# Kernel tuning notes

Hardware: AMD Instinct MI355X
Metric: run time of the kernel (lower is better)

Reference implementation:

```python
import jax, jax.numpy as jnp
import numpy as np

HEADS = 4
HEAD_DIM = 32
NUM_GRAPHS = 512


def _transformer_conv(x, Wq, bq, Wk, bk, Wv, bv, Ws, bs, src, dst):
    # PyG TransformerConv, concat=False, root_weight=True, beta=False, eval mode (no dropout).
    N = x.shape[0]
    q = (x @ Wq + bq).reshape(N, HEADS, HEAD_DIM)
    k = (x @ Wk + bk).reshape(N, HEADS, HEAD_DIM)
    v = (x @ Wv + bv).reshape(N, HEADS, HEAD_DIM)
    scale = 1.0 / np.sqrt(HEAD_DIM).astype(np.float32)
    # per-edge attention logits: query at target (dst), key at source (src)
    logits = jnp.einsum('ehd,ehd->eh', q[dst], k[src]) * scale  # [E, H]
    # segment softmax over incoming edges of each target node
    m = jax.ops.segment_max(logits, dst, num_segments=N)        # [N, H]
    p = jnp.exp(logits - m[dst])                                # [E, H]
    denom = jax.ops.segment_sum(p, dst, num_segments=N)         # [N, H]
    a = p / jnp.maximum(denom[dst], 1e-16)                      # [E, H]
    msg = a[:, :, None] * v[src]                                # [E, H, D]
    out = jax.ops.segment_sum(msg, dst, num_segments=N)         # [N, H, D]
    out = out.mean(axis=1)                                      # concat=False -> head mean
    return out + (x @ Ws + bs)                                  # root/skip connection


def _global_mean_pool(x, batch, num_graphs):
    s = jax.ops.segment_sum(x, batch, num_segments=num_graphs)
    cnt = jax.ops.segment_sum(jnp.ones((x.shape[0],), x.dtype), batch, num_segments=num_graphs)
    return s / jnp.maximum(cnt, 1.0)[:, None]


def setup_inputs() -> dict:
    key = jax.random.key(0)
    ks = jax.random.split(key, 20)
    N, E, C, H = 100000, 1600000, 128, 32
    d = {
        'x': jax.random.normal(ks[0], (N, C), jnp.float32),
        'edge_index': jax.random.randint(ks[1], (2, E), 0, N, jnp.int64),
        'batch': jnp.sort(jax.random.randint(ks[2], (N,), 0, NUM_GRAPHS, jnp.int64)),
    }
    def lin(k, fan_in, fan_out):
        lim = 1.0 / np.sqrt(fan_in)
        k1, k2 = jax.random.split(k)
        return (jax.random.uniform(k1, (fan_in, fan_out), jnp.float32, -lim, lim),
                jax.random.uniform(k2, (fan_out,), jnp.float32, -lim, lim))
    d['Wq1'], d['bq1'] = lin(ks[3], C, HEADS * HEAD_DIM)
    d['Wk1'], d['bk1'] = lin(ks[4], C, HEADS * HEAD_DIM)
    d['Wv1'], d['bv1'] = lin(ks[5], C, HEADS * HEAD_DIM)
    d['Ws1'], d['bs1'] = lin(ks[6], C, H)
    d['Wq2'], d['bq2'] = lin(ks[7], H, HEADS * HEAD_DIM)
    d['Wk2'], d['bk2'] = lin(ks[8], H, HEADS * HEAD_DIM)
    d['Wv2'], d['bv2'] = lin(ks[9], H, HEADS * HEAD_DIM)
    d['Ws2'], d['bs2'] = lin(ks[10], H, H)
    return d


def reference(x, edge_index, batch, Wq1, bq1, Wk1, bk1, Wv1, bv1, Ws1, bs1,
              Wq2, bq2, Wk2, bk2, Wv2, bv2, Ws2, bs2):
    src, dst = edge_index[0], edge_index[1]
    h = _transformer_conv(x, Wq1, bq1, Wk1, bk1, Wv1, bv1, Ws1, bs1, src, dst)
    h = jax.nn.relu(h)
    h = _transformer_conv(h, Wq2, bq2, Wk2, bk2, Wv2, bv2, Ws2, bs2, src, dst)
    h = jax.nn.relu(h)
    return _global_mean_pool(h, batch, NUM_GRAPHS)
```

## Files before the change

### kernel.cpp

```cpp
#include <hip/hip_runtime.h>
#include <math.h>

typedef __attribute__((ext_vector_type(8))) short bf16x8;
typedef __attribute__((ext_vector_type(4))) float f32x4;

__device__ __forceinline__ float b2f(unsigned short u) {
    union { unsigned u32; float f; } x; x.u32 = (unsigned)u << 16; return x.f;
}
__device__ __forceinline__ unsigned short f2b(float f) {
    union { float f; unsigned u32; } x; x.f = f;
    unsigned u = x.u32;
    unsigned r = (u + 0x7fffu + ((u >> 16) & 1u)) >> 16;
    return (unsigned short)r;
}

__device__ __forceinline__ unsigned char f2e4m3(float f) {
    union { float f; unsigned u; } x; x.f = f;
    unsigned s = (x.u >> 24) & 0x80;
    x.u &= 0x7fffffff;
    if (!(x.f == x.f)) return (unsigned char)(s | 0x7e);
    if (x.f >= 448.f) return (unsigned char)(s | 0x7e);
    if (x.f < 0.015625f) {
        int m = (int)rintf(x.f * 512.f);
        if (m >= 8) return (unsigned char)(s | 0x08);
        return (unsigned char)(s | (unsigned)m);
    }
    unsigned exp = x.u >> 23;
    unsigned mant = x.u & 0x7fffff;
    unsigned m3 = mant >> 20;
    unsigned rb = (mant >> 19) & 1u;
    unsigned sticky = (mant & 0x7ffffu) ? 1u : 0u;
    m3 += rb & (sticky | (m3 & 1u));
    if (m3 == 8) { m3 = 0; exp++; }
    unsigned e4 = exp - 120;
    if (e4 >= 15 && m3 > 6) { e4 = 15; m3 = 6; }
    return (unsigned char)(s | (e4 << 3) | m3);
}

__device__ __forceinline__ void acc4_fp8(float exs, unsigned vw, float4& acc) {
    union { unsigned u; float f; } t;
    t.u = ((vw & 0x80u) << 24) | ((vw & 0x7fu) << 20);        acc.x += exs * t.f;
    t.u = ((vw & 0x8000u) << 16) | ((vw & 0x7f00u) << 12);    acc.y += exs * t.f;
    t.u = ((vw & 0x800000u) << 8) | ((vw & 0x7f0000u) << 4);  acc.z += exs * t.f;
    t.u = (vw & 0x80000000u) | ((vw & 0x7f000000u) >> 4);     acc.w += exs * t.f;
}

__device__ __forceinline__ f32x4 mfma16(bf16x8 a, bf16x8 b, f32x4 c) {
    return __builtin_amdgcn_mfma_f32_16x16x32_bf16(a, b, c, 0, 0, 0);
}

__device__ __forceinline__ void async_copy16(const unsigned* g, void* l) {
    __builtin_amdgcn_global_load_lds(
        (const __attribute__((address_space(1))) unsigned*)g,
        (__attribute__((address_space(3))) unsigned*)l, 16, 0, 0);
}


__global__ __launch_bounds__(256) void hist_k(const int* __restrict__ dst, int* __restrict__ deg, int E) {
    int e = blockIdx.x * 256 + threadIdx.x;
    if (e < E) atomicAdd(&deg[dst[e]], 1);
}

__global__ __launch_bounds__(256) void scanA_k(const int* __restrict__ deg, int* __restrict__ rowptr,
                                               int* __restrict__ partials, int N) {
    __shared__ int sh[256];
    int t = threadIdx.x;
    int base = blockIdx.x * 1024 + t * 4;
    int v0 = 0, v1 = 0, v2 = 0, v3 = 0;
    if (base + 0 < N) v0 = deg[base + 0];
    if (base + 1 < N) v1 = deg[base + 1];
    if (base + 2 < N) v2 = deg[base + 2];
    if (base + 3 < N) v3 = deg[base + 3];
    sh[t] = v0 + v1 + v2 + v3;
    __syncthreads();
    for (int off = 1; off < 256; off <<= 1) {
        int add = (t >= off) ? sh[t - off] : 0;
        __syncthreads();
        sh[t] += add;
        __syncthreads();
    }
    int run = (t > 0) ? sh[t - 1] : 0;
    if (base + 0 < N) rowptr[base + 0] = run; run += v0;
    if (base + 1 < N) rowptr[base + 1] = run; run += v1;
    if (base + 2 < N) rowptr[base + 2] = run; run += v2;
    if (base + 3 < N) rowptr[base + 3] = run;
    if (t == 255) partials[blockIdx.x] = sh[255];
}

__global__ void scanB_k(int* partials, int nch) {
    if (threadIdx.x == 0 && blockIdx.x == 0) {
        int run = 0;
        for (int i = 0; i < nch; ++i) { int x = partials[i]; partials[i] = run; run += x; }
        partials[nch] = run;
    }
}

__global__ __launch_bounds__(256) void addoff_k(int* __restrict__ rowptr, const int* __restrict__ partials,
                                                int N, int nch) {
    int t = threadIdx.x;
    int off = partials[blockIdx.x];
    int base = blockIdx.x * 1024;
    for (int i = 0; i < 4; ++i) {
        int idx = base + t + i * 256;
        if (idx < N) rowptr[idx] += off;
    }
    if (blockIdx.x == 0 && t == 0) rowptr[N] = partials[nch];
}

__global__ __launch_bounds__(256) void scatter_k(const int* __restrict__ src, const int* __restrict__ dst,
                                                 const int* __restrict__ rowptr, int* __restrict__ cnt,
                                                 int* __restrict__ srcid, int E) {
    int e = blockIdx.x * 256 + threadIdx.x;
    if (e < E) {
        int d = dst[e];
        int pos = rowptr[d] + atomicAdd(&cnt[d], 1);
        srcid[pos] = src[e];
    }
}


__global__ __launch_bounds__(256) void cvt_k(const float* __restrict__ x,
                                             unsigned short* __restrict__ hi,
                                             unsigned short* __restrict__ lo, long n4) {
    long stride = (long)gridDim.x * 256;
    for (long i = (long)blockIdx.x * 256 + threadIdx.x; i < n4; i += stride) {
        float4 v = ((const float4*)x)[i];
        ushort4 h, L;
        h.x = f2b(v.x); L.x = f2b(v.x - b2f(h.x));
        h.y = f2b(v.y); L.y = f2b(v.y - b2f(h.y));
        h.z = f2b(v.z); L.z = f2b(v.z - b2f(h.z));
        h.w = f2b(v.w); L.w = f2b(v.w - b2f(h.w));
        ((ushort4*)hi)[i] = h;
        ((ushort4*)lo)[i] = L;
    }
}


__global__ __launch_bounds__(256) void wprep_k(
    const float* __restrict__ Wq, const float* __restrict__ Wk,
    const float* __restrict__ Wv, const float* __restrict__ Ws,
    int ksteps, unsigned* __restrict__ fhi, unsigned* __restrict__ flo)
{
    int idx = blockIdx.x * 256 + threadIdx.x;
    int total = 26 * ksteps * 64 * 4;
    if (idx >= total) return;
    int w = idx & 3;
    int lane = (idx >> 2) & 63;
    int tmp = idx >> 8;
    int kk = tmp % ksteps;
    int t = tmp / ksteps;
    int col = t * 16 + (lane & 15);
    int k0 = kk * 32 + ((lane >> 4) << 3) + (w << 1);
    const float* W; int ow, c;
    if (col < 128)      { W = Wq; ow = 128; c = col; }
    else if (col < 256) { W = Wk; ow = 128; c = col - 128; }
    else if (col < 384) { W = Wv; ow = 128; c = col - 256; }
    else                { W = Ws; ow = 32;  c = col - 384; }
    float v0 = W[(size_t)k0 * ow + c];
    float v1 = W[(size_t)(k0 + 1) * ow + c];
    unsigned short h0 = f2b(v0), h1 = f2b(v1);
    unsigned short l0 = f2b(v0 - b2f(h0)), l1 = f2b(v1 - b2f(h1));
    fhi[idx] = (unsigned)h0 | ((unsigned)h1 << 16);
    flo[idx] = (unsigned)l0 | ((unsigned)l1 << 16);
}


template<int KSTEPS>
__global__ __launch_bounds__(1024) void qkvs_mfma(const unsigned short* __restrict__ Xhi,
    const unsigned short* __restrict__ Xlo, int Cin, int N,
    const unsigned* __restrict__ fhi, const unsigned* __restrict__ flo,
    const float* __restrict__ bq, const float* __restrict__ bk,
    const float* __restrict__ bv, const float* __restrict__ bs,
    unsigned short* __restrict__ q, unsigned char* __restrict__ kvb,
    float* __restrict__ sk, int rtPer)
{
    constexpr int NT = 7;
    constexpr int NIDX = KSTEPS * NT * 2 * 64;
    __shared__ float4 ldsB[NIDX];

    int tid = threadIdx.x;
    int lane = tid & 63, wid = tid >> 6;
    int tbase = blockIdx.y * NT;

    for (int u = tid; u < NIDX; u += 1024) {
        int l = u & 63;
        int rest = u >> 6;
        int plane = rest & 1;
        int tt = (rest >> 1) % NT;
        int kk = (rest >> 1) / NT;
        if (tbase + tt < 26) {
            const unsigned* srcp = plane ? flo : fhi;
            size_t so = (((size_t)(tbase + tt) * KSTEPS + kk) * 64 + l) * 4;
            async_copy16(srcp + so, &ldsB[u - l]);
        }
    }
    __syncthreads();

    const int asub = (lane >> 4) << 3;
    int rtTotal = (N + 15) >> 4;
    int rtStart = blockIdx.x * rtPer;
    int rtEnd = rtStart + rtPer; if (rtEnd > rtTotal) rtEnd = rtTotal;

    for (int rt = rtStart + wid; rt < rtEnd; rt += 16) {
        int row = rt * 16 + (lane & 15);
        int rowc = row < N ? row : N - 1;
        const unsigned short* xh = Xhi + (size_t)rowc * Cin + asub;
        const unsigned short* xl = Xlo + (size_t)rowc * Cin + asub;

        f32x4 acc[NT];
#pragma unroll
        for (int t = 0; t < NT; ++t) acc[t] = (f32x4){0.f, 0.f, 0.f, 0.f};

        bf16x8 ah = *(const bf16x8*)xh;
        bf16x8 al = *(const bf16x8*)xl;
#pragma unroll
        for (int kk = 0; kk < KSTEPS; ++kk) {
            bf16x8 ahn, aln;
            if (kk + 1 < KSTEPS) {
                ahn = *(const bf16x8*)(xh + (kk + 1) * 32);
                aln = *(const bf16x8*)(xl + (kk + 1) * 32);
            }
            const float4* base = &ldsB[kk * NT * 2 * 64];
#pragma unroll
            for (int t = 0; t < NT; ++t) {
                bf16x8 bh = *(const bf16x8*)&base[(t * 2 + 0) * 64 + lane];
                bf16x8 bl = *(const bf16x8*)&base[(t * 2 + 1) * 64 + lane];
                acc[t] = mfma16(ah, bh, acc[t]);
                acc[t] = mfma16(al, bh, acc[t]);
                acc[t] = mfma16(ah, bl, acc[t]);
            }
            if (kk + 1 < KSTEPS) { ah = ahn; al = aln; }
        }

#pragma unroll
        for (int t = 0; t < NT; ++t) {
            int col = (tbase + t) * 16 + (lane & 15);
            if (col >= 416) continue;
            int sel; const float* bp; int c;
            if (col < 128)      { sel = 0; bp = bq; c = col; }
            else if (col < 256) { sel = 1; bp = bk; c = col - 128; }
            else if (col < 384) { sel = 2; bp = bv; c = col - 256; }
            else                { sel = 3; bp = bs; c = col - 384; }
            float bias = bp[c];
#pragma unroll
            for (int r = 0; r < 4; ++r) {
                int orow = rt * 16 + ((lane >> 4) << 2) + r;
                if (orow >= N) continue;
                float val = acc[t][r] + bias;
                if (sel == 0)      q[(size_t)orow * 128 + c] = f2b(val);
                else if (sel == 1) *(unsigned short*)(kvb + (size_t)orow * 384 + c * 2) = f2b(val);
                else if (sel == 2) kvb[(size_t)orow * 384 + 256 + c] = f2e4m3(val);
                else               sk[(size_t)orow * 32 + c] = val;
            }
        }
    }
}


__global__ __launch_bounds__(256) void attn_k(const unsigned short* __restrict__ q,
    const unsigned char* __restrict__ kv,
    const float* __restrict__ sk,
    const int* __restrict__ rowptr, const int* __restrict__ srcid,
    float* __restrict__ outF, unsigned short* __restrict__ outHi,
    unsigned short* __restrict__ outLo, int mode, int N)
{
    int grp = threadIdx.x >> 5;
    int n = blockIdx.x * 8 + grp;
    if (n >= N) return;
    int l = threadIdx.x & 31;
    int s = l & 7;
    const float c2 = 0.25504233001306574f;

    ushort4 qr = *(const ushort4*)(q + (size_t)n * 128 + l * 4);
    float4 qv = make_float4(b2f(qr.x), b2f(qr.y), b2f(qr.z), b2f(qr.w));
    float4 acc = make_float4(0.f, 0.f, 0.f, 0.f);
    float lsum = 0.f;

    int e0 = rowptr[n], e1 = rowptr[n + 1];
    int e = e0;
    for (; e + 4 <= e1; e += 4) {
        int s0 = srcid[e], s1 = srcid[e + 1], s2 = srcid[e + 2], s3 = srcid[e + 3];
        const unsigned char* b0 = kv + (size_t)s0 * 384;
        const unsigned char* b1 = kv + (size_t)s1 * 384;
        const unsigned char* b2 = kv + (size_t)s2 * 384;
        const unsigned char* b3 = kv + (size_t)s3 * 384;
        ushort4 k0 = *(const ushort4*)(b0 + (l << 3));
        ushort4 k1 = *(const ushort4*)(b1 + (l << 3));
        ushort4 k2 = *(const ushort4*)(b2 + (l << 3));
        ushort4 k3 = *(const ushort4*)(b3 + (l << 3));
        unsigned vw0 = *(const unsigned*)(b0 + 256 + (l << 2));
        unsigned vw1 = *(const unsigned*)(b1 + 256 + (l << 2));
        unsigned vw2 = *(const unsigned*)(b2 + 256 + (l << 2));
        unsigned vw3 = *(const unsigned*)(b3 + 256 + (l << 2));

        float p0 = qv.x * b2f(k0.x) + qv.y * b2f(k0.y) + qv.z * b2f(k0.z) + qv.w * b2f(k0.w);
        float p1 = qv.x * b2f(k1.x) + qv.y * b2f(k1.y) + qv.z * b2f(k1.z) + qv.w * b2f(k1.w);
        float p2 = qv.x * b2f(k2.x) + qv.y * b2f(k2.y) + qv.z * b2f(k2.z) + qv.w * b2f(k2.w);
        float p3 = qv.x * b2f(k3.x) + qv.y * b2f(k3.y) + qv.z * b2f(k3.z) + qv.w * b2f(k3.w);
        p0 += __shfl_xor(p0, 1, 8); p0 += __shfl_xor(p0, 2, 8); p0 += __shfl_xor(p0, 4, 8);
        p1 += __shfl_xor(p1, 1, 8); p1 += __shfl_xor(p1, 2, 8); p1 += __shfl_xor(p1, 4, 8);
        p2 += __shfl_xor(p2, 1, 8); p2 += __shfl_xor(p2, 2, 8); p2 += __shfl_xor(p2, 4, 8);
        p3 += __shfl_xor(p3, 1, 8); p3 += __shfl_xor(p3, 2, 8); p3 += __shfl_xor(p3, 4, 8);
        float ex0 = exp2f(fminf(p0 * c2, 86.f));
        float ex1 = exp2f(fminf(p1 * c2, 86.f));
        float ex2 = exp2f(fminf(p2 * c2, 86.f));
        float ex3 = exp2f(fminf(p3 * c2, 86.f));
        lsum += (ex0 + ex1) + (ex2 + ex3);
        acc4_fp8(ex0 * 0x1p120f, vw0, acc);
        acc4_fp8(ex1 * 0x1p120f, vw1, acc);
        acc4_fp8(ex2 * 0x1p120f, vw2, acc);
        acc4_fp8(ex3 * 0x1p120f, vw3, acc);
    }
    for (; e < e1; ++e) {
        const unsigned char* b0 = kv + (size_t)srcid[e] * 384;
        ushort4 k0 = *(const ushort4*)(b0 + (l << 3));
        unsigned vw0 = *(const unsigned*)(b0 + 256 + (l << 2));
        float p0 = qv.x * b2f(k0.x) + qv.y * b2f(k0.y) + qv.z * b2f(k0.z) + qv.w * b2f(k0.w);
        p0 += __shfl_xor(p0, 1, 8); p0 += __shfl_xor(p0, 2, 8); p0 += __shfl_xor(p0, 4, 8);
        float ex0 = exp2f(fminf(p0 * c2, 86.f));
        lsum += ex0;
        acc4_fp8(ex0 * 0x1p120f, vw0, acc);
    }

    float inv = 0.25f / fmaxf(lsum, 1e-16f);
    float rx = acc.x * inv, ry = acc.y * inv, rz = acc.z * inv, rw = acc.w * inv;
    rx += __shfl_xor(rx, 8, 32);  rx += __shfl_xor(rx, 16, 32);
    ry += __shfl_xor(ry, 8, 32);  ry += __shfl_xor(ry, 16, 32);
    rz += __shfl_xor(rz, 8, 32);  rz += __shfl_xor(rz, 16, 32);
    rw += __shfl_xor(rw, 8, 32);  rw += __shfl_xor(rw, 16, 32);

    if (l < 8) {
        const float* skp = sk + (size_t)n * 32 + s * 4;
        float o0 = fmaxf(rx + skp[0], 0.f), o1 = fmaxf(ry + skp[1], 0.f);
        float o2 = fmaxf(rz + skp[2], 0.f), o3 = fmaxf(rw + skp[3], 0.f);
        if (mode == 0) {
            *(float4*)(outF + (size_t)n * 32 + s * 4) = make_float4(o0, o1, o2, o3);
        } else {
            ushort4 h, L;
            h.x = f2b(o0); L.x = f2b(o0 - b2f(h.x));
            h.y = f2b(o1); L.y = f2b(o1 - b2f(h.y));
            h.z = f2b(o2); L.z = f2b(o2 - b2f(h.z));
            h.w = f2b(o3); L.w = f2b(o3 - b2f(h.w));
            *(ushort4*)(outHi + (size_t)n * 32 + s * 4) = h;
            *(ushort4*)(outLo + (size_t)n * 32 + s * 4) = L;
        }
    }
}


__global__ __launch_bounds__(256) void pool_k(const float* __restrict__ h, const int* __restrict__ batch,
                                              float* __restrict__ out, int N)
{
    int g = blockIdx.x;
    int t = threadIdx.x;
    int lo = 0, hi = N;
    while (lo < hi) { int mid = (lo + hi) >> 1; if (batch[mid] < g) lo = mid + 1; else hi = mid; }
    int start = lo;
    lo = 0; hi = N;
    while (lo < hi) { int mid = (lo + hi) >> 1; if (batch[mid] < g + 1) lo = mid + 1; else hi = mid; }
    int end = lo;
    int c = t & 31, r0 = t >> 5;
    float s = 0.f;
    for (int r = start + r0; r < end; r += 8) s += h[(size_t)r * 32 + c];
    __shared__ float sh[256];
    sh[t] = s;
    __syncthreads();
    if (t < 32) {
        float tot = sh[t] + sh[t + 32] + sh[t + 64] + sh[t + 96]
                  + sh[t + 128] + sh[t + 160] + sh[t + 192] + sh[t + 224];
        float cnt = (float)(end - start);
        out[(size_t)g * 32 + t] = tot / fmaxf(cnt, 1.f);
    }
}


extern "C" void kernel_launch(void* const* d_in, const int* in_sizes, int n_in,
                              void* d_out, int out_size, void* d_ws, size_t ws_size,
                              hipStream_t stream) {
    const float* x   = (const float*)d_in[0];
    const int* ei    = (const int*)d_in[1];
    const int* batch = (const int*)d_in[2];
    const float *Wq1 = (const float*)d_in[3],  *bq1 = (const float*)d_in[4];
    const float *Wk1 = (const float*)d_in[5],  *bk1 = (const float*)d_in[6];
    const float *Wv1 = (const float*)d_in[7],  *bv1 = (const float*)d_in[8];
    const float *Ws1 = (const float*)d_in[9],  *bs1 = (const float*)d_in[10];
    const float *Wq2 = (const float*)d_in[11], *bq2 = (const float*)d_in[12];
    const float *Wk2 = (const float*)d_in[13], *bk2 = (const float*)d_in[14];
    const float *Wv2 = (const float*)d_in[15], *bv2 = (const float*)d_in[16];
    const float *Ws2 = (const float*)d_in[17], *bs2 = (const float*)d_in[18];
    float* out = (float*)d_out;

    int N = in_sizes[0] / 128;
    int E = in_sizes[1] / 2;
    const int* src = ei;
    const int* dst = ei + E;

    char* ws = (char*)d_ws;
    size_t off = 0;
    auto alloc = [&](size_t bytes) -> void* {
        void* p = ws + off;
        off += (bytes + 255) & ~(size_t)255;
        return p;
    };
    int* deg      = (int*)alloc((size_t)N * 4);
    int* cnt      = (int*)alloc((size_t)N * 4);
    int* rowptr   = (int*)alloc(((size_t)N + 1) * 4);
    int* partials = (int*)alloc(4096);
    int* srcid    = (int*)alloc((size_t)E * 4);
    unsigned* fhi1 = (unsigned*)alloc(26 * 4 * 64 * 4 * 4);
    unsigned* flo1 = (unsigned*)alloc(26 * 4 * 64 * 4 * 4);
    unsigned* fhi2 = (unsigned*)alloc(26 * 1 * 64 * 4 * 4);
    unsigned* flo2 = (unsigned*)alloc(26 * 1 * 64 * 4 * 4);
    unsigned short* Xhi = (unsigned short*)alloc((size_t)N * 128 * 2);
    unsigned short* Xlo = (unsigned short*)alloc((size_t)N * 128 * 2);
    unsigned short* q   = (unsigned short*)alloc((size_t)N * 128 * 2);
    unsigned char* kvb  = (unsigned char*)alloc((size_t)N * 384);
    float* sk     = (float*)alloc((size_t)N * 32 * 4);
    unsigned short* h1hi = (unsigned short*)alloc((size_t)N * 32 * 2);
    unsigned short* h1lo = (unsigned short*)alloc((size_t)N * 32 * 2);
    float* h2     = (float*)alloc((size_t)N * 32 * 4);

    hipMemsetAsync(deg, 0, (size_t)N * 4, stream);
    hipMemsetAsync(cnt, 0, (size_t)N * 4, stream);

    int nch = (N + 1023) / 1024;
    hist_k<<<(E + 255) / 256, 256, 0, stream>>>(dst, deg, E);
    scanA_k<<<nch, 256, 0, stream>>>(deg, rowptr, partials, N);
    scanB_k<<<1, 64, 0, stream>>>(partials, nch);
    addoff_k<<<nch, 256, 0, stream>>>(rowptr, partials, N, nch);
    scatter_k<<<(E + 255) / 256, 256, 0, stream>>>(src, dst, rowptr, cnt, srcid, E);

    wprep_k<<<(26 * 4 * 64 * 4 + 255) / 256, 256, 0, stream>>>(Wq1, Wk1, Wv1, Ws1, 4, fhi1, flo1);
    wprep_k<<<(26 * 1 * 64 * 4 + 255) / 256, 256, 0, stream>>>(Wq2, Wk2, Wv2, Ws2, 1, fhi2, flo2);
    cvt_k<<<2048, 256, 0, stream>>>(x, Xhi, Xlo, (long)N * 32);

    int rtTotal = (N + 15) / 16;
    int rtPer = (rtTotal + 127) / 128;
    dim3 gq(128, 4);
    qkvs_mfma<4><<<gq, 1024, 0, stream>>>(Xhi, Xlo, 128, N, fhi1, flo1,
        bq1, bk1, bv1, bs1, q, kvb, sk, rtPer);
    attn_k<<<(N + 7) / 8, 256, 0, stream>>>(q, kvb, sk, rowptr, srcid,
        nullptr, h1hi, h1lo, 1, N);
    qkvs_mfma<1><<<gq, 1024, 0, stream>>>(h1hi, h1lo, 32, N, fhi2, flo2,
        bq2, bk2, bv2, bs2, q, kvb, sk, rtPer);
    attn_k<<<(N + 7) / 8, 256, 0, stream>>>(q, kvb, sk, rowptr, srcid,
        h2, nullptr, nullptr, 0, N);
    pool_k<<<512, 256, 0, stream>>>(h2, batch, out, N);
}
```

Measured before the change: 558.0 us.

## Interleave hi/lo bf16 planes, fuse prep kernels, prefetch next row tile in GEMM

Merges the degree histogram, input bf16 hi/lo split and both weight-prep launches into one multi-role kernel to cut launch count. The hi and lo bf16 planes of X and h1 are stored interleaved per 8-element group, so each row's A operand for hi and lo comes from adjacent addresses. The QKVS MFMA loop now loads the whole next row tile's A fragments into registers before computing the current one, which raises register pressure. The attention kernel writes its layer-1 output in the same interleaved layout.

```diff
diff --git a/kernel.cpp b/kernel.cpp
--- a/kernel.cpp
+++ b/kernel.cpp
@@ -55,11 +55,6 @@
         (__attribute__((address_space(3))) unsigned*)l, 16, 0, 0);
 }
 
-
-__global__ __launch_bounds__(256) void hist_k(const int* __restrict__ dst, int* __restrict__ deg, int E) {
-    int e = blockIdx.x * 256 + threadIdx.x;
-    if (e < E) atomicAdd(&deg[dst[e]], 1);
-}
 
 __global__ __launch_bounds__(256) void scanA_k(const int* __restrict__ deg, int* __restrict__ rowptr,
                                                int* __restrict__ partials, int N) {
@@ -119,31 +114,58 @@
 }
 
 
-__global__ __launch_bounds__(256) void cvt_k(const float* __restrict__ x,
-                                             unsigned short* __restrict__ hi,
-                                             unsigned short* __restrict__ lo, long n4) {
-    long stride = (long)gridDim.x * 256;
-    for (long i = (long)blockIdx.x * 256 + threadIdx.x; i < n4; i += stride) {
-        float4 v = ((const float4*)x)[i];
-        ushort4 h, L;
-        h.x = f2b(v.x); L.x = f2b(v.x - b2f(h.x));
-        h.y = f2b(v.y); L.y = f2b(v.y - b2f(h.y));
-        h.z = f2b(v.z); L.z = f2b(v.z - b2f(h.z));
-        h.w = f2b(v.w); L.w = f2b(v.w - b2f(h.w));
-        ((ushort4*)hi)[i] = h;
-        ((ushort4*)lo)[i] = L;
-    }
-}
-
-
-__global__ __launch_bounds__(256) void wprep_k(
-    const float* __restrict__ Wq, const float* __restrict__ Wk,
-    const float* __restrict__ Wv, const float* __restrict__ Ws,
-    int ksteps, unsigned* __restrict__ fhi, unsigned* __restrict__ flo)
+__global__ __launch_bounds__(256) void prep_k(
+    const int* __restrict__ dst, int* __restrict__ deg, int E, int histB,
+    const float* __restrict__ x, unsigned short* __restrict__ Xc, int ngrp, int cvtB,
+    const float* __restrict__ Wq1, const float* __restrict__ Wk1,
+    const float* __restrict__ Wv1, const float* __restrict__ Ws1,
+    unsigned* __restrict__ fhi1, unsigned* __restrict__ flo1, int w1B,
+    const float* __restrict__ Wq2, const float* __restrict__ Wk2,
+    const float* __restrict__ Wv2, const float* __restrict__ Ws2,
+    unsigned* __restrict__ fhi2, unsigned* __restrict__ flo2)
 {
-    int idx = blockIdx.x * 256 + threadIdx.x;
-    int total = 26 * ksteps * 64 * 4;
-    if (idx >= total) return;
+    int b = blockIdx.x;
+    int tid = threadIdx.x;
+    if (b < histB) {
+        int e = b * 256 + tid;
+        if (e < E) atomicAdd(&deg[dst[e]], 1);
+        return;
+    }
+    b -= histB;
+    if (b < cvtB) {
+        int gi = b * 256 + tid;
+        if (gi < ngrp) {
+            const float* xp = x + (size_t)gi * 8;
+            float4 a0 = *(const float4*)xp;
+            float4 a1 = *(const float4*)(xp + 4);
+            unsigned short* op = Xc + (size_t)gi * 16;
+            ushort4 h0, h1, L0, L1;
+            h0.x = f2b(a0.x); L0.x = f2b(a0.x - b2f(h0.x));
+            h0.y = f2b(a0.y); L0.y = f2b(a0.y - b2f(h0.y));
+            h0.z = f2b(a0.z); L0.z = f2b(a0.z - b2f(h0.z));
+            h0.w = f2b(a0.w); L0.w = f2b(a0.w - b2f(h0.w));
+            h1.x = f2b(a1.x); L1.x = f2b(a1.x - b2f(h1.x));
+            h1.y = f2b(a1.y); L1.y = f2b(a1.y - b2f(h1.y));
+            h1.z = f2b(a1.z); L1.z = f2b(a1.z - b2f(h1.z));
+            h1.w = f2b(a1.w); L1.w = f2b(a1.w - b2f(h1.w));
+            *(ushort4*)(op)      = h0;
+            *(ushort4*)(op + 4)  = h1;
+            *(ushort4*)(op + 8)  = L0;
+            *(ushort4*)(op + 12) = L1;
+        }
+        return;
+    }
+    b -= cvtB;
+    const float *Wq, *Wk, *Wv, *Ws; unsigned *fhi, *flo; int ksteps, idx;
+    if (b < w1B) {
+        Wq = Wq1; Wk = Wk1; Wv = Wv1; Ws = Ws1; fhi = fhi1; flo = flo1;
+        ksteps = 4; idx = b * 256 + tid;
+        if (idx >= 26 * 4 * 64 * 4) return;
+    } else {
+        Wq = Wq2; Wk = Wk2; Wv = Wv2; Ws = Ws2; fhi = fhi2; flo = flo2;
+        ksteps = 1; idx = (b - w1B) * 256 + tid;
+        if (idx >= 26 * 1 * 64 * 4) return;
+    }
     int w = idx & 3;
     int lane = (idx >> 2) & 63;
     int tmp = idx >> 8;
@@ -166,8 +188,8 @@
 
 
 template<int KSTEPS>
-__global__ __launch_bounds__(1024) void qkvs_mfma(const unsigned short* __restrict__ Xhi,
-    const unsigned short* __restrict__ Xlo, int Cin, int N,
+__global__ __launch_bounds__(1024) void qkvs_mfma(const unsigned short* __restrict__ Xc,
+    int Cin, int N,
     const unsigned* __restrict__ fhi, const unsigned* __restrict__ flo,
     const float* __restrict__ bq, const float* __restrict__ bk,
     const float* __restrict__ bv, const float* __restrict__ bs,
@@ -196,31 +218,40 @@
     }
     __syncthreads();
 
-    const int asub = (lane >> 4) << 3;
+    const int asub2 = ((lane >> 4) << 3) * 2;
+    const int rowStride = 2 * Cin;
     int rtTotal = (N + 15) >> 4;
     int rtStart = blockIdx.x * rtPer;
     int rtEnd = rtStart + rtPer; if (rtEnd > rtTotal) rtEnd = rtTotal;
 
-    for (int rt = rtStart + wid; rt < rtEnd; rt += 16) {
-        int row = rt * 16 + (lane & 15);
+    auto loadA = [&](int rtX, bf16x8* dstA) {
+        int row = rtX * 16 + (lane & 15);
         int rowc = row < N ? row : N - 1;
-        const unsigned short* xh = Xhi + (size_t)rowc * Cin + asub;
-        const unsigned short* xl = Xlo + (size_t)rowc * Cin + asub;
+        const unsigned short* xp = Xc + (size_t)rowc * rowStride + asub2;
+#pragma unroll
+        for (int kk = 0; kk < KSTEPS; ++kk) {
+            dstA[2 * kk]     = *(const bf16x8*)(xp + kk * 64);
+            dstA[2 * kk + 1] = *(const bf16x8*)(xp + kk * 64 + 8);
+        }
+    };
+
+    bf16x8 aCur[2 * KSTEPS];
+    int rt0 = rtStart + wid;
+    if (rt0 < rtEnd) loadA(rt0, aCur);
+
+    for (int rt = rt0; rt < rtEnd; rt += 16) {
+        bf16x8 aNxt[2 * KSTEPS];
+        bool hasNext = (rt + 16) < rtEnd;
+        if (hasNext) loadA(rt + 16, aNxt);
 
         f32x4 acc[NT];
 #pragma unroll
         for (int t = 0; t < NT; ++t) acc[t] = (f32x4){0.f, 0.f, 0.f, 0.f};
 
-        bf16x8 ah = *(const bf16x8*)xh;
-        bf16x8 al = *(const bf16x8*)xl;
 #pragma unroll
         for (int kk = 0; kk < KSTEPS; ++kk) {
-            bf16x8 ahn, aln;
-            if (kk + 1 < KSTEPS) {
-                ahn = *(const bf16x8*)(xh + (kk + 1) * 32);
-                aln = *(const bf16x8*)(xl + (kk + 1) * 32);
-            }
             const float4* base = &ldsB[kk * NT * 2 * 64];
+            bf16x8 ah = aCur[2 * kk], al = aCur[2 * kk + 1];
 #pragma unroll
             for (int t = 0; t < NT; ++t) {
                 bf16x8 bh = *(const bf16x8*)&base[(t * 2 + 0) * 64 + lane];
@@ -229,7 +260,6 @@
                 acc[t] = mfma16(al, bh, acc[t]);
                 acc[t] = mfma16(ah, bl, acc[t]);
             }
-            if (kk + 1 < KSTEPS) { ah = ahn; al = aln; }
         }
 
 #pragma unroll
@@ -253,6 +283,11 @@
                 else               sk[(size_t)orow * 32 + c] = val;
             }
         }
+
+        if (hasNext) {
+#pragma unroll
+            for (int i = 0; i < 2 * KSTEPS; ++i) aCur[i] = aNxt[i];
+        }
     }
 }
 
@@ -261,8 +296,7 @@
     const unsigned char* __restrict__ kv,
     const float* __restrict__ sk,
     const int* __restrict__ rowptr, const int* __restrict__ srcid,
-    float* __restrict__ outF, unsigned short* __restrict__ outHi,
-    unsigned short* __restrict__ outLo, int mode, int N)
+    float* __restrict__ outF, unsigned short* __restrict__ outC, int mode, int N)
 {
     int grp = threadIdx.x >> 5;
     int n = blockIdx.x * 8 + grp;
@@ -341,8 +375,9 @@
             h.y = f2b(o1); L.y = f2b(o1 - b2f(h.y));
             h.z = f2b(o2); L.z = f2b(o2 - b2f(h.z));
             h.w = f2b(o3); L.w = f2b(o3 - b2f(h.w));
-            *(ushort4*)(outHi + (size_t)n * 32 + s * 4) = h;
-            *(ushort4*)(outLo + (size_t)n * 32 + s * 4) = L;
+            unsigned short* op = outC + (size_t)n * 64 + (s >> 1) * 16 + (s & 1) * 4;
+            *(ushort4*)op       = h;
+            *(ushort4*)(op + 8) = L;
         }
     }
 }
@@ -411,39 +446,43 @@
     unsigned* flo1 = (unsigned*)alloc(26 * 4 * 64 * 4 * 4);
     unsigned* fhi2 = (unsigned*)alloc(26 * 1 * 64 * 4 * 4);
     unsigned* flo2 = (unsigned*)alloc(26 * 1 * 64 * 4 * 4);
-    unsigned short* Xhi = (unsigned short*)alloc((size_t)N * 128 * 2);
-    unsigned short* Xlo = (unsigned short*)alloc((size_t)N * 128 * 2);
+    unsigned short* Xc  = (unsigned short*)alloc((size_t)N * 256 * 2);
     unsigned short* q   = (unsigned short*)alloc((size_t)N * 128 * 2);
     unsigned char* kvb  = (unsigned char*)alloc((size_t)N * 384);
     float* sk     = (float*)alloc((size_t)N * 32 * 4);
-    unsigned short* h1hi = (unsigned short*)alloc((size_t)N * 32 * 2);
-    unsigned short* h1lo = (unsigned short*)alloc((size_t)N * 32 * 2);
+    unsigned short* h1c = (unsigned short*)alloc((size_t)N * 64 * 2);
     float* h2     = (float*)alloc((size_t)N * 32 * 4);
 
     hipMemsetAsync(deg, 0, (size_t)N * 4, stream);
     hipMemsetAsync(cnt, 0, (size_t)N * 4, stream);
 
+    int histB = (E + 255) / 256;
+    int ngrp = N * 16;
+    int cvtB = (ngrp + 255) / 256;
+    int w1B = (26 * 4 * 64 * 4 + 255) / 256;
+    int w2B = (26 * 1 * 64 * 4 + 255) / 256;
+    prep_k<<<histB + cvtB + w1B + w2B, 256, 0, stream>>>(
+        dst, deg, E, histB,
+        x, Xc, ngrp, cvtB,
+        Wq1, Wk1, Wv1, Ws1, fhi1, flo1, w1B,
+        Wq2, Wk2, Wv2, Ws2, fhi2, flo2);
+
     int nch = (N + 1023) / 1024;
-    hist_k<<<(E + 255) / 256, 256, 0, stream>>>(dst, deg, E);
     scanA_k<<<nch, 256, 0, stream>>>(deg, rowptr, partials, N);
     scanB_k<<<1, 64, 0, stream>>>(partials, nch);
     addoff_k<<<nch, 256, 0, stream>>>(rowptr, partials, N, nch);
     scatter_k<<<(E + 255) / 256, 256, 0, stream>>>(src, dst, rowptr, cnt, srcid, E);
 
-    wprep_k<<<(26 * 4 * 64 * 4 + 255) / 256, 256, 0, stream>>>(Wq1, Wk1, Wv1, Ws1, 4, fhi1, flo1);
-    wprep_k<<<(26 * 1 * 64 * 4 + 255) / 256, 256, 0, stream>>>(Wq2, Wk2, Wv2, Ws2, 1, fhi2, flo2);
-    cvt_k<<<2048, 256, 0, stream>>>(x, Xhi, Xlo, (long)N * 32);
-
     int rtTotal = (N + 15) / 16;
     int rtPer = (rtTotal + 127) / 128;
     dim3 gq(128, 4);
-    qkvs_mfma<4><<<gq, 1024, 0, stream>>>(Xhi, Xlo, 128, N, fhi1, flo1,
+    qkvs_mfma<4><<<gq, 1024, 0, stream>>>(Xc, 128, N, fhi1, flo1,
         bq1, bk1, bv1, bs1, q, kvb, sk, rtPer);
     attn_k<<<(N + 7) / 8, 256, 0, stream>>>(q, kvb, sk, rowptr, srcid,
-        nullptr, h1hi, h1lo, 1, N);
-    qkvs_mfma<1><<<gq, 1024, 0, stream>>>(h1hi, h1lo, 32, N, fhi2, flo2,
+        nullptr, h1c, 1, N);
+    qkvs_mfma<1><<<gq, 1024, 0, stream>>>(h1c, 32, N, fhi2, flo2,
         bq2, bk2, bv2, bs2, q, kvb, sk, rtPer);
     attn_k<<<(N + 7) / 8, 256, 0, stream>>>(q, kvb, sk, rowptr, srcid,
-        h2, nullptr, nullptr, 0, N);
+        h2, nullptr, 0, N);
     pool_k<<<512, 256, 0, stream>>>(h2, batch, out, N);
 }
```

Result: faster. 524.5 us (-6.0%).
